# Performance work log

Hardware: AMD Instinct MI355X
Metric: run time of the kernel (lower is better)

Reference implementation:

```python
import jax, jax.numpy as jnp
import numpy as np

NUM_HEADS = 8

def setup_inputs() -> dict:
    key = jax.random.key(0)
    ks = jax.random.split(key, 12)
    T, B, C, D = 2048, 4, 512, 512
    s = 1.0 / np.sqrt(C)
    return {
        "key_in": jax.random.normal(ks[0], (T, B, C), jnp.float32),
        "value_in": jax.random.normal(ks[1], (T, B, C), jnp.float32),
        "query_in": jax.random.normal(ks[2], (T, B, C), jnp.float32),
        "Wk": jax.random.normal(ks[3], (C, D), jnp.float32) * s,
        "bk": jax.random.normal(ks[4], (D,), jnp.float32) * 0.01,
        "Wv": jax.random.normal(ks[5], (C, D), jnp.float32) * s,
        "bv": jax.random.normal(ks[6], (D,), jnp.float32) * 0.01,
        "Wq": jax.random.normal(ks[7], (C, D), jnp.float32) * s,
        "bq": jax.random.normal(ks[8], (D,), jnp.float32) * 0.01,
        "Wo": jax.random.normal(ks[9], (D, D), jnp.float32) * (1.0 / np.sqrt(D)),
        "bo": jax.random.normal(ks[10], (D,), jnp.float32) * 0.01,
    }

def reference(key_in, value_in, query_in, Wk, bk, Wv, bv, Wq, bq, Wo, bo):
    T, B, C = query_in.shape
    D = Wq.shape[1]
    H = NUM_HEADS
    hd = D // H
    scale = 1.0 / np.sqrt(hd).astype(np.float32)
    # Linear projections on (T, B, C) -> (T, B, D), then the original's
    # row-major view(B, -1, H, hd) followed by transpose(1, 2) -> (B, H, T, hd)
    def proj(x, W, b):
        y = x @ W + b                      # (T, B, D)
        return y.reshape(B, -1, H, hd).transpose(0, 2, 1, 3)  # (B, H, T, hd)
    q = proj(query_in, Wq, bq)
    k = proj(key_in, Wk, bk)
    v = proj(value_in, Wv, bv)
    scores = jnp.einsum("bhqd,bhkd->bhqk", q, k) * scale  # (B, H, T, T)
    attn = jax.nn.softmax(scores, axis=-1)
    x = jnp.einsum("bhqk,bhkd->bhqd", attn, v)            # (B, H, T, hd)
    x = x.transpose(0, 2, 1, 3).reshape(T, B, D)          # matches .view(T, B, d_model)
    return x @ Wo + bo
```

## Files before the change

### kernel.cpp

```cpp
#include <hip/hip_runtime.h>
#include <math.h>

#define MROWS 8192
#define DM    512
#define SEQL  2048
#define HDIM  64
#define NSPLIT 2

typedef __attribute__((ext_vector_type(4))) float floatx4;
typedef _Float16 half2v __attribute__((ext_vector_type(2)));
typedef _Float16 half4v __attribute__((ext_vector_type(4)));
typedef _Float16 half8v __attribute__((ext_vector_type(8)));

#define CEXP 0.18033688011f

__device__ __forceinline__ void gll16(const void* g, void* l) {
    __builtin_amdgcn_global_load_lds(
        (const __attribute__((address_space(1))) unsigned int*)g,
        (__attribute__((address_space(3))) unsigned int*)l, 16, 0, 0);
}

__device__ __forceinline__ half4v pack4(float a, float b, float c, float d) {
    half2v lo = __builtin_bit_cast(half2v, __builtin_amdgcn_cvt_pkrtz(a, b));
    half2v hi = __builtin_bit_cast(half2v, __builtin_amdgcn_cvt_pkrtz(c, d));
    half4v r;
    r[0] = lo[0]; r[1] = lo[1]; r[2] = hi[0]; r[3] = hi[1];
    return r;
}

__global__ __launch_bounds__(256) void transw(const float* __restrict__ w0,
                                              const float* __restrict__ w1,
                                              const float* __restrict__ w2,
                                              const float* __restrict__ w3,
                                              _Float16* __restrict__ t0,
                                              _Float16* __restrict__ t1,
                                              _Float16* __restrict__ t2,
                                              _Float16* __restrict__ t3) {
    __shared__ float tile[32][33];
    const float* W = blockIdx.z == 0 ? w0 : (blockIdx.z == 1 ? w1 : (blockIdx.z == 2 ? w2 : w3));
    _Float16* T = blockIdx.z == 0 ? t0 : (blockIdx.z == 1 ? t1 : (blockIdx.z == 2 ? t2 : t3));
    const float sc = (blockIdx.z == 0) ? CEXP : 1.0f;
    const int tx = threadIdx.x & 31, ty = threadIdx.x >> 5;
    const int x = blockIdx.x * 32 + tx;
    const int y0 = blockIdx.y * 32;
#pragma unroll
    for (int i = 0; i < 4; ++i)
        tile[ty + i * 8][tx] = W[(size_t)(y0 + ty + i * 8) * DM + x];
    __syncthreads();
    const int xo = y0 + tx;
#pragma unroll
    for (int i = 0; i < 4; ++i)
        T[(size_t)(blockIdx.x * 32 + ty + i * 8) * DM + xo] = (_Float16)(tile[tx][ty + i * 8] * sc);
}

__global__ __launch_bounds__(256, 3) void proj_gemm(
        const float* __restrict__ q32, const float* __restrict__ k32, const float* __restrict__ v32,
        const _Float16* __restrict__ Wq, const _Float16* __restrict__ Wk, const _Float16* __restrict__ Wv,
        const float* __restrict__ bq, const float* __restrict__ bk, const float* __restrict__ bv,
        _Float16* __restrict__ Qo, _Float16* __restrict__ Ko, _Float16* __restrict__ Vto) {
    __shared__ _Float16 Bs[512 * 32];
    __shared__ _Float16 As[32 * 32];
    const int z = blockIdx.y;
    const float* A32    = z == 0 ? q32 : (z == 1 ? k32 : v32);
    const _Float16* Bt  = z == 0 ? Wq : (z == 1 ? Wk : Wv);
    const float* bias   = z == 0 ? bq : (z == 1 ? bk : bv);
    const float bscale  = z == 0 ? CEXP : 1.0f;

    const int tid = threadIdx.x;
    const int w = tid >> 6;
    const int l15 = tid & 15, quad = (tid & 63) >> 4;
    const int m0 = blockIdx.x * 32;

    floatx4 acc[2][8];
#pragma unroll
    for (int i = 0; i < 2; ++i)
#pragma unroll
        for (int j = 0; j < 8; ++j) acc[i][j] = (floatx4){0.f, 0.f, 0.f, 0.f};

    for (int kt = 0; kt < DM / 32; ++kt) {
        __syncthreads();
#pragma unroll
        for (int i = 0; i < 8; ++i) {
            const int c = i * 256 + tid;
            const int row = c >> 2, g = c & 3;
            const int kg = g ^ (row & 3);
            gll16(&Bt[(size_t)row * DM + kt * 32 + kg * 8], &Bs[c * 8]);
        }
        if (tid < 128) {
            const int c = tid;
            const int row = c >> 2, g = c & 3;
            const int kg = g ^ (row & 3);
            const float* src = &A32[(size_t)(m0 + row) * DM + kt * 32 + kg * 8];
            const float4 f0 = *(const float4*)&src[0];
            const float4 f1 = *(const float4*)&src[4];
            half8v o;
            o[0] = (_Float16)f0.x; o[1] = (_Float16)f0.y; o[2] = (_Float16)f0.z; o[3] = (_Float16)f0.w;
            o[4] = (_Float16)f1.x; o[5] = (_Float16)f1.y; o[6] = (_Float16)f1.z; o[7] = (_Float16)f1.w;
            *(half8v*)&As[c * 8] = o;
        }
        __syncthreads();
        half8v af[2], bfr[8];
#pragma unroll
        for (int i = 0; i < 2; ++i) {
            const int row = i * 16 + l15;
            af[i] = *(const half8v*)&As[row * 32 + (quad ^ (row & 3)) * 8];
        }
#pragma unroll
        for (int j = 0; j < 8; ++j) {
            const int row = w * 128 + j * 16 + l15;
            bfr[j] = *(const half8v*)&Bs[row * 32 + (quad ^ (row & 3)) * 8];
        }
#pragma unroll
        for (int i = 0; i < 2; ++i)
#pragma unroll
            for (int j = 0; j < 8; ++j)
                acc[i][j] = __builtin_amdgcn_mfma_f32_16x16x32_f16(af[i], bfr[j], acc[i][j], 0, 0, 0);
    }
#pragma unroll
    for (int j = 0; j < 8; ++j) {
        const int col = w * 128 + j * 16 + l15;
        const float bv4 = bias[col] * bscale;
#pragma unroll
        for (int i = 0; i < 2; ++i) {
            const int rb = m0 + i * 16 + quad * 4;
            if (z == 2) {
                const int g = rb >> 11, seq = rb & 2047;
                half4v pv;
#pragma unroll
                for (int r = 0; r < 4; ++r) pv[r] = (_Float16)(acc[i][j][r] + bv4);
                *(half4v*)&Vto[((size_t)g * DM + col) * SEQL + seq] = pv;
            } else {
                _Float16* oh = z == 0 ? Qo : Ko;
#pragma unroll
                for (int r = 0; r < 4; ++r)
                    oh[(size_t)(rb + r) * DM + col] = (_Float16)(acc[i][j][r] + bv4);
            }
        }
    }
}

__global__ __launch_bounds__(256, 4) void out_gemm(
        const _Float16* __restrict__ Op0, const _Float16* __restrict__ Op1,
        const float* __restrict__ lp,
        const _Float16* __restrict__ Wo, const float* __restrict__ bo,
        float* __restrict__ out) {
    __shared__ _Float16 Bs[256 * 64];
    __shared__ _Float16 As[32 * 64];
    const int tid = threadIdx.x;
    const int w = tid >> 6;
    const int l15 = tid & 15, quad = (tid & 63) >> 4;
    const int n0 = blockIdx.x * 256, m0 = blockIdx.y * 32;

    floatx4 acc[2][4];
#pragma unroll
    for (int i = 0; i < 2; ++i)
#pragma unroll
        for (int j = 0; j < 4; ++j) acc[i][j] = (floatx4){0.f, 0.f, 0.f, 0.f};

    for (int kt = 0; kt < DM / 64; ++kt) {
        __syncthreads();
#pragma unroll
        for (int i = 0; i < 8; ++i) {
            const int c = i * 256 + tid;
            const int row = c >> 3, g = c & 7;
            const int kg = g ^ (row & 7);
            gll16(&Wo[(size_t)(n0 + row) * DM + kt * 64 + kg * 8], &Bs[c * 8]);
        }
        {
            const int c = tid;
            const int row = c >> 3, g = c & 7;
            const int kg = g ^ (row & 7);
            const int grow = m0 + row;
            const size_t off = (size_t)grow * DM + kt * 64 + kg * 8;
            const half8v a = *(const half8v*)&Op0[off];
            const half8v b = *(const half8v*)&Op1[off];
            const float inv = 1.0f / (lp[(size_t)grow * 8 + kt] +
                                      lp[((size_t)MROWS + grow) * 8 + kt]);
            half8v s;
#pragma unroll
            for (int e = 0; e < 8; ++e)
                s[e] = (_Float16)(((float)a[e] + (float)b[e]) * inv);
            *(half8v*)&As[c * 8] = s;
        }
        __syncthreads();
#pragma unroll
        for (int ks = 0; ks < 2; ++ks) {
            half8v af[2], bfr[4];
#pragma unroll
            for (int i = 0; i < 2; ++i) {
                const int row = i * 16 + l15;
                af[i] = *(const half8v*)&As[row * 64 + ((ks * 4 + quad) ^ (row & 7)) * 8];
            }
#pragma unroll
            for (int j = 0; j < 4; ++j) {
                const int row = w * 64 + j * 16 + l15;
                bfr[j] = *(const half8v*)&Bs[row * 64 + ((ks * 4 + quad) ^ (row & 7)) * 8];
            }
#pragma unroll
            for (int i = 0; i < 2; ++i)
#pragma unroll
                for (int j = 0; j < 4; ++j)
                    acc[i][j] = __builtin_amdgcn_mfma_f32_16x16x32_f16(af[i], bfr[j], acc[i][j], 0, 0, 0);
        }
    }
#pragma unroll
    for (int j = 0; j < 4; ++j) {
        const int col = n0 + w * 64 + j * 16 + l15;
        const float bv4 = bo[col];
#pragma unroll
        for (int i = 0; i < 2; ++i) {
            const int rb = m0 + i * 16 + quad * 4;
#pragma unroll
            for (int r = 0; r < 4; ++r)
                out[(size_t)(rb + r) * DM + col] = acc[i][j][r] + bv4;
        }
    }
}

__global__ __launch_bounds__(256, 4) void attn_mfma(const _Float16* __restrict__ Q16,
                                                    const _Float16* __restrict__ K16,
                                                    const _Float16* __restrict__ Vt,
                                                    _Float16* __restrict__ Opart,
                                                    float* __restrict__ lpart) {
    __shared__ _Float16 Ks[2][64 * 64];
    __shared__ _Float16 Vs[2][64 * 64];

    const int tid  = threadIdx.x;
    const int lane = tid & 63;
    const int l15  = lane & 15;
    const int quad = lane >> 4;

    const int pair  = blockIdx.y;
    const int split = blockIdx.z;
    const int grp   = pair >> 3;
    const int h     = pair & 7;
    const int q0    = blockIdx.x * 128;
    const int rQ    = grp * SEQL + q0 + (tid >> 6) * 32;
    const int cb    = h * HDIM;
    const int NIT   = (SEQL / 64) / NSPLIT;
    const int kt0   = split * NIT;

    const _Float16* Kbase = K16 + (size_t)grp * SEQL * DM + cb;
    const _Float16* Vbase = Vt + (size_t)grp * DM * SEQL + (size_t)cb * SEQL;

    half8v qf[2][2];
#pragma unroll
    for (int qt = 0; qt < 2; ++qt)
#pragma unroll
        for (int ks = 0; ks < 2; ++ks)
            qf[qt][ks] = *(const half8v*)&Q16[(size_t)(rQ + qt * 16 + l15) * DM + cb + ks * 32 + quad * 8];

    floatx4 oacc[2][4], lacc[2];
#pragma unroll
    for (int qt = 0; qt < 2; ++qt) {
        lacc[qt] = (floatx4){0.f, 0.f, 0.f, 0.f};
#pragma unroll
        for (int dt = 0; dt < 4; ++dt) oacc[qt][dt] = (floatx4){0.f, 0.f, 0.f, 0.f};
    }
    half4v ones;
    ones[0] = (_Float16)1.f; ones[1] = (_Float16)1.f; ones[2] = (_Float16)1.f; ones[3] = (_Float16)1.f;

#define STAGE(KT, B)                                                            \
    {                                                                           \
        _Float16* ksb = &Ks[B][0];                                              \
        _Float16* vsb = &Vs[B][0];                                              \
        _Pragma("unroll")                                                       \
        for (int i_ = 0; i_ < 4; ++i_) {                                        \
            const int c_ = i_ * 256 + tid;                                      \
            if (c_ < 512) {                                                     \
                const int key_ = c_ >> 3, g_ = c_ & 7;                          \
                const int dg_ = g_ ^ (key_ & 7);                                \
                gll16(&Kbase[(size_t)((KT) * 64 + key_) * DM + dg_ * 8],        \
                      &ksb[c_ * 8]);                                            \
            } else {                                                            \
                const int cv_ = c_ - 512;                                       \
                const int d_ = cv_ >> 3, g_ = cv_ & 7;                          \
                const int kg_ = g_ ^ (d_ & 7);                                  \
                gll16(&Vbase[(size_t)d_ * SEQL + (KT) * 64 + kg_ * 8],          \
                      &vsb[cv_ * 8]);                                           \
            }                                                                   \
        }                                                                       \
    }

    STAGE(kt0, 0)

    for (int it = 0; it < NIT; ++it) {
        const int cur = it & 1;
        __syncthreads();
        if (it + 1 < NIT) STAGE(kt0 + it + 1, cur ^ 1)

        const _Float16* ksb = &Ks[cur][0];
        const _Float16* vsb = &Vs[cur][0];

        floatx4 st[4][2];
#pragma unroll
        for (int ktile = 0; ktile < 4; ++ktile) {
            const int key = ktile * 16 + l15;
            const half8v kf0 = *(const half8v*)&ksb[key * 64 + ((0 + quad) ^ (key & 7)) * 8];
            const half8v kf1 = *(const half8v*)&ksb[key * 64 + ((4 + quad) ^ (key & 7)) * 8];
#pragma unroll
            for (int qt = 0; qt < 2; ++qt) {
                floatx4 z = {0.f, 0.f, 0.f, 0.f};
                z = __builtin_amdgcn_mfma_f32_16x16x32_f16(kf0, qf[qt][0], z, 0, 0, 0);
                st[ktile][qt] = __builtin_amdgcn_mfma_f32_16x16x32_f16(kf1, qf[qt][1], z, 0, 0, 0);
            }
        }

        half4v pa[4][2];
#pragma unroll
        for (int ktile = 0; ktile < 4; ++ktile)
#pragma unroll
            for (int qt = 0; qt < 2; ++qt)
                pa[ktile][qt] = pack4(__builtin_amdgcn_exp2f(st[ktile][qt][0]),
                                      __builtin_amdgcn_exp2f(st[ktile][qt][1]),
                                      __builtin_amdgcn_exp2f(st[ktile][qt][2]),
                                      __builtin_amdgcn_exp2f(st[ktile][qt][3]));

#pragma unroll
        for (int qt = 0; qt < 2; ++qt)
#pragma unroll
            for (int ktile = 0; ktile < 4; ++ktile)
                lacc[qt] = __builtin_amdgcn_mfma_f32_16x16x16f16(pa[ktile][qt], ones, lacc[qt], 0, 0, 0);

#pragma unroll
        for (int dt = 0; dt < 4; ++dt) {
            const int d = dt * 16 + l15;
#pragma unroll
            for (int ktile = 0; ktile < 4; ++ktile) {
                const int G = ktile * 2 + (quad >> 1);
                const int slot = G ^ (d & 7);
                const half4v vf = *(const half4v*)&vsb[d * 64 + slot * 8 + (quad & 1) * 4];
#pragma unroll
                for (int qt = 0; qt < 2; ++qt)
                    oacc[qt][dt] = __builtin_amdgcn_mfma_f32_16x16x16f16(pa[ktile][qt], vf, oacc[qt][dt], 0, 0, 0);
            }
        }
    }

    _Float16* Op = Opart + (size_t)split * MROWS * DM;
#pragma unroll
    for (int qt = 0; qt < 2; ++qt)
#pragma unroll
        for (int r = 0; r < 4; ++r) {
            const int qrow = rQ + qt * 16 + quad * 4 + r;
            const size_t rowoff = (size_t)qrow * DM + cb;
#pragma unroll
            for (int dt = 0; dt < 4; ++dt)
                Op[rowoff + dt * 16 + l15] = (_Float16)oacc[qt][dt][r];
            if (l15 == 0)
                lpart[((size_t)split * MROWS + qrow) * 8 + h] = lacc[qt][r];
        }
}

extern "C" void kernel_launch(void* const* d_in, const int* in_sizes, int n_in,
                              void* d_out, int out_size, void* d_ws, size_t ws_size,
                              hipStream_t stream) {
    const float* key_in   = (const float*)d_in[0];
    const float* value_in = (const float*)d_in[1];
    const float* query_in = (const float*)d_in[2];
    const float* Wk = (const float*)d_in[3];
    const float* bk = (const float*)d_in[4];
    const float* Wv = (const float*)d_in[5];
    const float* bv = (const float*)d_in[6];
    const float* Wq = (const float*)d_in[7];
    const float* bq = (const float*)d_in[8];
    const float* Wo = (const float*)d_in[9];
    const float* bo = (const float*)d_in[10];
    float* out = (float*)d_out;

    const size_t MAT = (size_t)MROWS * DM;
    _Float16* Q16  = (_Float16*)d_ws;
    _Float16* K16  = Q16 + MAT;
    _Float16* Vtb  = K16 + MAT;
    _Float16* Wqt  = Vtb + MAT;
    _Float16* Wkt  = Wqt + DM * DM;
    _Float16* Wvt  = Wkt + DM * DM;
    _Float16* Wot  = Wvt + DM * DM;
    float*    lpart = (float*)(Wot + DM * DM);
    _Float16* Opart = (_Float16*)(lpart + 2 * MROWS * 8);

    const dim3 blk(256);

    transw<<<dim3(16, 16, 4), blk, 0, stream>>>(Wq, Wk, Wv, Wo, Wqt, Wkt, Wvt, Wot);

    proj_gemm<<<dim3(MROWS / 32, 3), blk, 0, stream>>>(
        query_in, key_in, value_in, Wqt, Wkt, Wvt, bq, bk, bv, Q16, K16, Vtb);

    attn_mfma<<<dim3(SEQL / 128, 32, NSPLIT), blk, 0, stream>>>(Q16, K16, Vtb, Opart, lpart);

    out_gemm<<<dim3(2, MROWS / 32), blk, 0, stream>>>(
        Opart, Opart + MAT, lpart, Wot, bo, out);
}
```

Measured before the change: 202.0 us.

## Double-buffer LDS tiles in projection and output GEMMs to overlap loads with MFMA

Both proj_gemm and out_gemm now use two LDS buffers for A and B. The next k-tile's global loads (global_load_lds for weights, register prefetch for activations) are issued before the MFMAs on the current tile, leaving one barrier per iteration instead of two. The A staging in proj_gemm is spread over all 256 threads as float4 loads. This doubles shared memory per block, so launch bounds drop to 2 blocks per CU, trading occupancy for latency hiding.

```diff
diff --git a/kernel.cpp b/kernel.cpp
--- a/kernel.cpp
+++ b/kernel.cpp
@@ -53,13 +53,13 @@
         T[(size_t)(blockIdx.x * 32 + ty + i * 8) * DM + xo] = (_Float16)(tile[tx][ty + i * 8] * sc);
 }
 
-__global__ __launch_bounds__(256, 3) void proj_gemm(
+__global__ __launch_bounds__(256, 2) void proj_gemm(
         const float* __restrict__ q32, const float* __restrict__ k32, const float* __restrict__ v32,
         const _Float16* __restrict__ Wq, const _Float16* __restrict__ Wk, const _Float16* __restrict__ Wv,
         const float* __restrict__ bq, const float* __restrict__ bk, const float* __restrict__ bv,
         _Float16* __restrict__ Qo, _Float16* __restrict__ Ko, _Float16* __restrict__ Vto) {
-    __shared__ _Float16 Bs[512 * 32];
-    __shared__ _Float16 As[32 * 32];
+    __shared__ _Float16 Bs[2][512 * 32];
+    __shared__ _Float16 As[2][32 * 32];
     const int z = blockIdx.y;
     const float* A32    = z == 0 ? q32 : (z == 1 ? k32 : v32);
     const _Float16* Bt  = z == 0 ? Wq : (z == 1 ? Wk : Wv);
@@ -71,50 +71,68 @@
     const int l15 = tid & 15, quad = (tid & 63) >> 4;
     const int m0 = blockIdx.x * 32;
 
+    const int arow = tid >> 3, ag = tid & 7;
+    const int acol = ((ag >> 1) ^ (arow & 3)) * 8 + (ag & 1) * 4;
+    const float* Ap = &A32[(size_t)(m0 + arow) * DM + acol];
+    const int adst = arow * 32 + ag * 4;
+
     floatx4 acc[2][8];
 #pragma unroll
     for (int i = 0; i < 2; ++i)
 #pragma unroll
         for (int j = 0; j < 8; ++j) acc[i][j] = (floatx4){0.f, 0.f, 0.f, 0.f};
 
+#define PROJ_STAGE_B(KT, BUF)                                                  \
+    _Pragma("unroll")                                                          \
+    for (int i_ = 0; i_ < 8; ++i_) {                                           \
+        const int c_ = i_ * 256 + tid;                                         \
+        const int row_ = c_ >> 2, g_ = c_ & 3;                                 \
+        const int kg_ = g_ ^ (row_ & 3);                                       \
+        gll16(&Bt[(size_t)row_ * DM + (KT) * 32 + kg_ * 8], &Bs[BUF][c_ * 8]); \
+    }
+
+    float4 areg = *(const float4*)Ap;
+    PROJ_STAGE_B(0, 0)
+    {
+        half4v h;
+        h[0] = (_Float16)areg.x; h[1] = (_Float16)areg.y;
+        h[2] = (_Float16)areg.z; h[3] = (_Float16)areg.w;
+        *(half4v*)&As[0][adst] = h;
+    }
+    __syncthreads();
+
     for (int kt = 0; kt < DM / 32; ++kt) {
-        __syncthreads();
-#pragma unroll
-        for (int i = 0; i < 8; ++i) {
-            const int c = i * 256 + tid;
-            const int row = c >> 2, g = c & 3;
-            const int kg = g ^ (row & 3);
-            gll16(&Bt[(size_t)row * DM + kt * 32 + kg * 8], &Bs[c * 8]);
-        }
-        if (tid < 128) {
-            const int c = tid;
-            const int row = c >> 2, g = c & 3;
-            const int kg = g ^ (row & 3);
-            const float* src = &A32[(size_t)(m0 + row) * DM + kt * 32 + kg * 8];
-            const float4 f0 = *(const float4*)&src[0];
-            const float4 f1 = *(const float4*)&src[4];
-            half8v o;
-            o[0] = (_Float16)f0.x; o[1] = (_Float16)f0.y; o[2] = (_Float16)f0.z; o[3] = (_Float16)f0.w;
-            o[4] = (_Float16)f1.x; o[5] = (_Float16)f1.y; o[6] = (_Float16)f1.z; o[7] = (_Float16)f1.w;
-            *(half8v*)&As[c * 8] = o;
-        }
-        __syncthreads();
+        const int cur = kt & 1;
+        const bool pf = (kt + 1 < DM / 32);
+        if (pf) {
+            areg = *(const float4*)(Ap + (size_t)(kt + 1) * 32);
+            PROJ_STAGE_B(kt + 1, cur ^ 1)
+        }
+        const _Float16* asb = As[cur];
+        const _Float16* bsb = Bs[cur];
         half8v af[2], bfr[8];
 #pragma unroll
         for (int i = 0; i < 2; ++i) {
             const int row = i * 16 + l15;
-            af[i] = *(const half8v*)&As[row * 32 + (quad ^ (row & 3)) * 8];
+            af[i] = *(const half8v*)&asb[row * 32 + (quad ^ (row & 3)) * 8];
         }
 #pragma unroll
         for (int j = 0; j < 8; ++j) {
             const int row = w * 128 + j * 16 + l15;
-            bfr[j] = *(const half8v*)&Bs[row * 32 + (quad ^ (row & 3)) * 8];
+            bfr[j] = *(const half8v*)&bsb[row * 32 + (quad ^ (row & 3)) * 8];
         }
 #pragma unroll
         for (int i = 0; i < 2; ++i)
 #pragma unroll
             for (int j = 0; j < 8; ++j)
                 acc[i][j] = __builtin_amdgcn_mfma_f32_16x16x32_f16(af[i], bfr[j], acc[i][j], 0, 0, 0);
+        if (pf) {
+            half4v h;
+            h[0] = (_Float16)areg.x; h[1] = (_Float16)areg.y;
+            h[2] = (_Float16)areg.z; h[3] = (_Float16)areg.w;
+            *(half4v*)&As[cur ^ 1][adst] = h;
+        }
+        __syncthreads();
     }
 #pragma unroll
     for (int j = 0; j < 8; ++j) {
@@ -139,62 +157,79 @@
     }
 }
 
-__global__ __launch_bounds__(256, 4) void out_gemm(
+__global__ __launch_bounds__(256, 2) void out_gemm(
         const _Float16* __restrict__ Op0, const _Float16* __restrict__ Op1,
         const float* __restrict__ lp,
         const _Float16* __restrict__ Wo, const float* __restrict__ bo,
         float* __restrict__ out) {
-    __shared__ _Float16 Bs[256 * 64];
-    __shared__ _Float16 As[32 * 64];
+    __shared__ _Float16 Bs[2][256 * 64];
+    __shared__ _Float16 As[2][32 * 64];
     const int tid = threadIdx.x;
     const int w = tid >> 6;
     const int l15 = tid & 15, quad = (tid & 63) >> 4;
     const int n0 = blockIdx.x * 256, m0 = blockIdx.y * 32;
 
+    const int arow = tid >> 3, ag = tid & 7;
+    const int akg = ag ^ (arow & 7);
+    const int grow = m0 + arow;
+    const size_t abase = (size_t)grow * DM + akg * 8;
+    const int adst = tid * 8;
+
     floatx4 acc[2][4];
 #pragma unroll
     for (int i = 0; i < 2; ++i)
 #pragma unroll
         for (int j = 0; j < 4; ++j) acc[i][j] = (floatx4){0.f, 0.f, 0.f, 0.f};
 
+#define OUT_STAGE_B(KT, BUF)                                                           \
+    _Pragma("unroll")                                                                  \
+    for (int i_ = 0; i_ < 8; ++i_) {                                                   \
+        const int c_ = i_ * 256 + tid;                                                 \
+        const int row_ = c_ >> 3, g_ = c_ & 7;                                         \
+        const int kg_ = g_ ^ (row_ & 7);                                               \
+        gll16(&Wo[(size_t)(n0 + row_) * DM + (KT) * 64 + kg_ * 8], &Bs[BUF][c_ * 8]);  \
+    }
+
+    half8v pa = *(const half8v*)&Op0[abase];
+    half8v pb = *(const half8v*)&Op1[abase];
+    float pl0 = lp[(size_t)grow * 8 + 0];
+    float pl1 = lp[((size_t)MROWS + grow) * 8 + 0];
+    OUT_STAGE_B(0, 0)
+    {
+        const float inv = 1.0f / (pl0 + pl1);
+        half8v s;
+#pragma unroll
+        for (int e = 0; e < 8; ++e)
+            s[e] = (_Float16)(((float)pa[e] + (float)pb[e]) * inv);
+        *(half8v*)&As[0][adst] = s;
+    }
+    __syncthreads();
+
     for (int kt = 0; kt < DM / 64; ++kt) {
-        __syncthreads();
-#pragma unroll
-        for (int i = 0; i < 8; ++i) {
-            const int c = i * 256 + tid;
-            const int row = c >> 3, g = c & 7;
-            const int kg = g ^ (row & 7);
-            gll16(&Wo[(size_t)(n0 + row) * DM + kt * 64 + kg * 8], &Bs[c * 8]);
-        }
-        {
-            const int c = tid;
-            const int row = c >> 3, g = c & 7;
-            const int kg = g ^ (row & 7);
-            const int grow = m0 + row;
-            const size_t off = (size_t)grow * DM + kt * 64 + kg * 8;
-            const half8v a = *(const half8v*)&Op0[off];
-            const half8v b = *(const half8v*)&Op1[off];
-            const float inv = 1.0f / (lp[(size_t)grow * 8 + kt] +
-                                      lp[((size_t)MROWS + grow) * 8 + kt]);
-            half8v s;
-#pragma unroll
-            for (int e = 0; e < 8; ++e)
-                s[e] = (_Float16)(((float)a[e] + (float)b[e]) * inv);
-            *(half8v*)&As[c * 8] = s;
-        }
-        __syncthreads();
+        const int cur = kt & 1;
+        const bool pf = (kt + 1 < DM / 64);
+        if (pf) {
+            const size_t off = abase + (size_t)(kt + 1) * 64;
+            pa = *(const half8v*)&Op0[off];
+            pb = *(const half8v*)&Op1[off];
+            pl0 = lp[(size_t)grow * 8 + (kt + 1)];
+            pl1 = lp[((size_t)MROWS + grow) * 8 + (kt + 1)];
+            OUT_STAGE_B(kt + 1, cur ^ 1)
+        }
+        const _Float16* asb = As[cur];
+        const _Float16* bsb = Bs[cur];
 #pragma unroll
         for (int ks = 0; ks < 2; ++ks) {
             half8v af[2], bfr[4];
 #pragma unroll
             for (int i = 0; i < 2; ++i) {
                 const int row = i * 16 + l15;
-                af[i] = *(const half8v*)&As[row * 64 + ((ks * 4 + quad) ^ (row & 7)) * 8];
+                af[i] = *(const half8v*)&asb[row * 64 + ((ks * 4 + quad) ^ (row & 7)) * 8];
             }
 #pragma unroll
             for (int j = 0; j < 4; ++j) {
                 const int row = w * 64 + j * 16 + l15;
-                bfr[j] = *(const half8v*)&Bs[row * 64 + ((ks * 4 + quad) ^ (row & 7)) * 8];
+                bfr[j] = *(const half8v*)&bsb[row * 64 + ((ks * 4 + quad) ^ (row & 7)) * 8];
             }
 #pragma unroll
             for (int i = 0; i < 2; ++i)
@@ -202,6 +237,15 @@
                 for (int j = 0; j < 4; ++j)
                     acc[i][j] = __builtin_amdgcn_mfma_f32_16x16x32_f16(af[i], bfr[j], acc[i][j], 0, 0, 0);
         }
+        if (pf) {
+            const float inv = 1.0f / (pl0 + pl1);
+            half8v s;
+#pragma unroll
+            for (int e = 0; e < 8; ++e)
+                s[e] = (_Float16)(((float)pa[e] + (float)pb[e]) * inv);
+            *(half8v*)&As[cur ^ 1][adst] = s;
+        }
+        __syncthreads();
     }
 #pragma unroll
     for (int j = 0; j < 4; ++j) {
```

New measurement: 225.3 us. 1.12x slower.

## Retile projection GEMM to 128x128 block tiles with 2x2 warp layout

Applied to the files above, without the earlier changes.

The QKV projection GEMM changes from 32-row by 512-column block tiles to 128x128 tiles with a K step of 64. The 4 warps are arranged 2x2, each computing a 64x64 sub-tile. Each block now reads a square tile, which improves arithmetic intensity and cuts redundant reloading of the full weight panel per 32 rows. In exchange, each fp32 activation row is read by 4 column blocks instead of 1, and the grid changes shape (64x4x3 blocks).

```diff
diff --git a/kernel.cpp b/kernel.cpp
--- a/kernel.cpp
+++ b/kernel.cpp
@@ -58,71 +58,83 @@
         const _Float16* __restrict__ Wq, const _Float16* __restrict__ Wk, const _Float16* __restrict__ Wv,
         const float* __restrict__ bq, const float* __restrict__ bk, const float* __restrict__ bv,
         _Float16* __restrict__ Qo, _Float16* __restrict__ Ko, _Float16* __restrict__ Vto) {
-    __shared__ _Float16 Bs[512 * 32];
-    __shared__ _Float16 As[32 * 32];
-    const int z = blockIdx.y;
+    __shared__ _Float16 As[128 * 64];
+    __shared__ _Float16 Bs[128 * 64];
+    const int z = blockIdx.z;
     const float* A32    = z == 0 ? q32 : (z == 1 ? k32 : v32);
     const _Float16* Bt  = z == 0 ? Wq : (z == 1 ? Wk : Wv);
     const float* bias   = z == 0 ? bq : (z == 1 ? bk : bv);
     const float bscale  = z == 0 ? CEXP : 1.0f;
 
     const int tid = threadIdx.x;
-    const int w = tid >> 6;
+    const int w = tid >> 6, wr = w >> 1, wc = w & 1;
     const int l15 = tid & 15, quad = (tid & 63) >> 4;
-    const int m0 = blockIdx.x * 32;
-
-    floatx4 acc[2][8];
-#pragma unroll
-    for (int i = 0; i < 2; ++i)
-#pragma unroll
-        for (int j = 0; j < 8; ++j) acc[i][j] = (floatx4){0.f, 0.f, 0.f, 0.f};
-
-    for (int kt = 0; kt < DM / 32; ++kt) {
+    const int m0 = blockIdx.x * 128, n0 = blockIdx.y * 128;
+
+    const int arow = tid >> 1, ah = tid & 1;
+    const float* Asrc = &A32[(size_t)(m0 + arow) * DM + ah * 32];
+    _Float16* Adst = &As[arow * 64];
+    const int asw = arow & 7;
+
+    floatx4 acc[4][4];
+#pragma unroll
+    for (int i = 0; i < 4; ++i)
+#pragma unroll
+        for (int j = 0; j < 4; ++j) acc[i][j] = (floatx4){0.f, 0.f, 0.f, 0.f};
+
+    for (int kt = 0; kt < DM / 64; ++kt) {
         __syncthreads();
-#pragma unroll
-        for (int i = 0; i < 8; ++i) {
+        floatx4 f[8];
+        {
+            const float* s = Asrc + (size_t)kt * 64;
+#pragma unroll
+            for (int q = 0; q < 8; ++q) f[q] = *(const floatx4*)&s[q * 4];
+        }
+#pragma unroll
+        for (int i = 0; i < 4; ++i) {
             const int c = i * 256 + tid;
-            const int row = c >> 2, g = c & 3;
-            const int kg = g ^ (row & 3);
-            gll16(&Bt[(size_t)row * DM + kt * 32 + kg * 8], &Bs[c * 8]);
-        }
-        if (tid < 128) {
-            const int c = tid;
-            const int row = c >> 2, g = c & 3;
-            const int kg = g ^ (row & 3);
-            const float* src = &A32[(size_t)(m0 + row) * DM + kt * 32 + kg * 8];
-            const float4 f0 = *(const float4*)&src[0];
-            const float4 f1 = *(const float4*)&src[4];
+            const int row = c >> 3, g = c & 7;
+            const int kg = g ^ (row & 7);
+            gll16(&Bt[(size_t)(n0 + row) * DM + kt * 64 + kg * 8], &Bs[c * 8]);
+        }
+#pragma unroll
+        for (int t = 0; t < 4; ++t) {
             half8v o;
-            o[0] = (_Float16)f0.x; o[1] = (_Float16)f0.y; o[2] = (_Float16)f0.z; o[3] = (_Float16)f0.w;
-            o[4] = (_Float16)f1.x; o[5] = (_Float16)f1.y; o[6] = (_Float16)f1.z; o[7] = (_Float16)f1.w;
-            *(half8v*)&As[c * 8] = o;
+            o[0] = (_Float16)f[2 * t][0]; o[1] = (_Float16)f[2 * t][1];
+            o[2] = (_Float16)f[2 * t][2]; o[3] = (_Float16)f[2 * t][3];
+            o[4] = (_Float16)f[2 * t + 1][0]; o[5] = (_Float16)f[2 * t + 1][1];
+            o[6] = (_Float16)f[2 * t + 1][2]; o[7] = (_Float16)f[2 * t + 1][3];
+            const int g = ah * 4 + t;
+            *(half8v*)&Adst[(g ^ asw) * 8] = o;
         }
         __syncthreads();
-        half8v af[2], bfr[8];
-#pragma unroll
-        for (int i = 0; i < 2; ++i) {
-            const int row = i * 16 + l15;
-            af[i] = *(const half8v*)&As[row * 32 + (quad ^ (row & 3)) * 8];
-        }
-#pragma unroll
-        for (int j = 0; j < 8; ++j) {
-            const int row = w * 128 + j * 16 + l15;
-            bfr[j] = *(const half8v*)&Bs[row * 32 + (quad ^ (row & 3)) * 8];
-        }
-#pragma unroll
-        for (int i = 0; i < 2; ++i)
-#pragma unroll
-            for (int j = 0; j < 8; ++j)
-                acc[i][j] = __builtin_amdgcn_mfma_f32_16x16x32_f16(af[i], bfr[j], acc[i][j], 0, 0, 0);
-    }
-#pragma unroll
-    for (int j = 0; j < 8; ++j) {
-        const int col = w * 128 + j * 16 + l15;
+#pragma unroll
+        for (int ks = 0; ks < 2; ++ks) {
+            half8v af[4], bf[4];
+#pragma unroll
+            for (int i = 0; i < 4; ++i) {
+                const int row = wr * 64 + i * 16 + l15;
+                af[i] = *(const half8v*)&As[row * 64 + (((ks * 4 + quad)) ^ (row & 7)) * 8];
+            }
+#pragma unroll
+            for (int j = 0; j < 4; ++j) {
+                const int row = wc * 64 + j * 16 + l15;
+                bf[j] = *(const half8v*)&Bs[row * 64 + (((ks * 4 + quad)) ^ (row & 7)) * 8];
+            }
+#pragma unroll
+            for (int i = 0; i < 4; ++i)
+#pragma unroll
+                for (int j = 0; j < 4; ++j)
+                    acc[i][j] = __builtin_amdgcn_mfma_f32_16x16x32_f16(af[i], bf[j], acc[i][j], 0, 0, 0);
+        }
+    }
+#pragma unroll
+    for (int j = 0; j < 4; ++j) {
+        const int col = n0 + wc * 64 + j * 16 + l15;
         const float bv4 = bias[col] * bscale;
 #pragma unroll
-        for (int i = 0; i < 2; ++i) {
-            const int rb = m0 + i * 16 + quad * 4;
+        for (int i = 0; i < 4; ++i) {
+            const int rb = m0 + wr * 64 + i * 16 + quad * 4;
             if (z == 2) {
                 const int g = rb >> 11, seq = rb & 2047;
                 half4v pv;
@@ -273,7 +285,7 @@
                 gll16(&Kbase[(size_t)((KT) * 64 + key_) * DM + dg_ * 8],        \
                       &ksb[c_ * 8]);                                            \
             } else {                                                            \
-                const int cv_ = c_ - 512;                                       \
+                const int cv_ = c_ - 512;                                      \
                 const int d_ = cv_ >> 3, g_ = cv_ & 7;                          \
                 const int kg_ = g_ ^ (d_ & 7);                                  \
                 gll16(&Vbase[(size_t)d_ * SEQL + (KT) * 64 + kg_ * 8],          \
@@ -383,7 +395,7 @@
 
     transw<<<dim3(16, 16, 4), blk, 0, stream>>>(Wq, Wk, Wv, Wo, Wqt, Wkt, Wvt, Wot);
 
-    proj_gemm<<<dim3(MROWS / 32, 3), blk, 0, stream>>>(
+    proj_gemm<<<dim3(MROWS / 128, DM / 128, 3), blk, 0, stream>>>(
         query_in, key_in, value_in, Wqt, Wkt, Wvt, bq, bk, bv, Q16, K16, Vtb);
 
     attn_mfma<<<dim3(SEQL / 128, 32, NSPLIT), blk, 0, stream>>>(Q16, K16, Vtb, Opart, lpart);
```

After: 200.0 us. No clear change (-1.0%).
